# Kernel optimization log

Hardware: AMD Instinct MI355X
Metric: run time of the kernel (lower is better)

The kernel has to match this reference:

```python
import jax, jax.numpy as jnp
import numpy as np


def setup_inputs() -> dict:
    key = jax.random.key(0)
    ks = jax.random.split(key, 9)
    B, C, D = 16384, 6, 128
    NUM_ITEMS, V0, V1 = 1_000_000, 1000, 50000
    init_range = 0.5 / D
    return {
        "central_items": jax.random.randint(ks[0], (B,), 0, NUM_ITEMS),
        "side_info0": jax.random.randint(ks[1], (B,), 0, V0),
        "side_info1": jax.random.randint(ks[2], (B, 5), 0, V1),
        "context_items": jax.random.randint(ks[3], (B, C), 0, NUM_ITEMS),
        "W_item_in": jax.random.uniform(ks[4], (NUM_ITEMS, D), jnp.float32, -init_range, init_range),
        "W_item_out": jax.random.uniform(ks[5], (NUM_ITEMS, D), jnp.float32, -init_range, init_range),
        "W_weights": jax.random.normal(ks[6], (NUM_ITEMS, 3), jnp.float32),
        "W_side0": jax.random.uniform(ks[7], (V0, D), jnp.float32, -init_range, init_range),
        "W_side1": jax.random.uniform(ks[8], (V1, D), jnp.float32, -init_range, init_range),
    }


def reference(central_items, side_info0, side_info1, context_items,
              W_item_in, W_item_out, W_weights, W_side0, W_side1):
    # _emb_items: gather item + side-info embeddings
    item_embs = W_item_in[central_items]              # [B, D]
    s0 = W_side0[side_info0]                          # [B, D]
    s1 = W_side1[side_info1].mean(axis=1)             # [B, 5, D] -> [B, D] (3D mean path)
    # cat + reshape(B, -1, D) == stack along a new axis since all have width D
    embs = jnp.stack([item_embs, s0, s1], axis=1)     # [B, K=3, D]
    w = jax.nn.softmax(W_weights[central_items], axis=1)  # [B, K]
    hidden = jnp.einsum("bk,bkd->bd", w, embs)        # softmax-weighted sum, [B, D]
    # scoring: bmm(hidden[B,1,D], context[B,D,C]) -> [B, C]
    ctx = W_item_out[context_items]                   # [B, C, D]
    logits = jnp.einsum("bd,bcd->bc", hidden, ctx)    # [B, C]
    return jax.nn.sigmoid(logits)
```

## Files before the change

kernel.cpp:

```cpp
#include <hip/hip_runtime.h>
#include <math.h>


#define B_CONST 16384
#define C_CONST 6
#define D_CONST 128

__global__ __launch_bounds__(256) void eges_kernel(
    const int* __restrict__ central,
    const int* __restrict__ side0,
    const int* __restrict__ side1,
    const int* __restrict__ ctx_items,
    const float* __restrict__ W_item_in,
    const float* __restrict__ W_item_out,
    const float* __restrict__ W_weights,
    const float* __restrict__ W_side0,
    const float* __restrict__ W_side1,
    float* __restrict__ out,
    int B)
{
    const int wave = threadIdx.x >> 6;
    const int lane = threadIdx.x & 63;
    const int b = (blockIdx.x << 2) + wave;
    if (b >= B) return;

    const int ci = central[b];

    const float* wp = &W_weights[(long long)ci * 3];
    float w0 = wp[0], w1 = wp[1], w2 = wp[2];
    float m = fmaxf(w0, fmaxf(w1, w2));
    float e0 = __expf(w0 - m), e1 = __expf(w1 - m), e2 = __expf(w2 - m);
    float inv = 1.0f / (e0 + e1 + e2);
    w0 = e0 * inv; w1 = e1 * inv; w2 = e2 * inv;

    const int d = lane * 2;

    float2 item = *(const float2*)&W_item_in[(long long)ci * D_CONST + d];
    float2 s0v  = *(const float2*)&W_side0[(long long)side0[b] * D_CONST + d];

    float sx = 0.f, sy = 0.f;
    #pragma unroll
    for (int j = 0; j < 5; ++j) {
        int i1 = side1[b * 5 + j];
        float2 t = *(const float2*)&W_side1[(long long)i1 * D_CONST + d];
        sx += t.x; sy += t.y;
    }
    sx *= 0.2f; sy *= 0.2f;

    const float hx = w0 * item.x + w1 * s0v.x + w2 * sx;
    const float hy = w0 * item.y + w1 * s0v.y + w2 * sy;

    #pragma unroll
    for (int c = 0; c < C_CONST; ++c) {
        int oi = ctx_items[b * C_CONST + c];
        float2 o = *(const float2*)&W_item_out[(long long)oi * D_CONST + d];
        float p = hx * o.x + hy * o.y;
        #pragma unroll
        for (int off = 32; off >= 1; off >>= 1)
            p += __shfl_xor(p, off, 64);
        if (lane == 0)
            out[b * C_CONST + c] = 1.0f / (1.0f + __expf(-p));
    }
}

extern "C" void kernel_launch(void* const* d_in, const int* in_sizes, int n_in,
                              void* d_out, int out_size, void* d_ws, size_t ws_size,
                              hipStream_t stream) {
    const int*   central    = (const int*)d_in[0];
    const int*   side0      = (const int*)d_in[1];
    const int*   side1      = (const int*)d_in[2];
    const int*   ctx_items  = (const int*)d_in[3];
    const float* W_item_in  = (const float*)d_in[4];
    const float* W_item_out = (const float*)d_in[5];
    const float* W_weights  = (const float*)d_in[6];
    const float* W_side0    = (const float*)d_in[7];
    const float* W_side1    = (const float*)d_in[8];
    float* out = (float*)d_out;

    const int B = in_sizes[0];
    const int blocks = (B + 3) / 4;

    eges_kernel<<<blocks, 256, 0, stream>>>(
        central, side0, side1, ctx_items,
        W_item_in, W_item_out, W_weights, W_side0, W_side1,
        out, B);
}
```

Before: 25.57 us.

## Process two batch rows per wave with float4 gathers and hoisted loads

Each 64-lane wave now handles two batch rows, one per 32-lane half, and each lane loads float4 chunks instead of float2. All index loads and all six context-row gathers are issued up front, before the softmax and dot products, so more memory requests are in flight at once. The shuffle reduction shrinks to 5 steps within a half-wave. This raises register use and depends on ctx_items rows being 8-byte aligned for the int2 loads, which holds since each row is 6 ints.

```diff
diff --git a/kernel.cpp b/kernel.cpp
--- a/kernel.cpp
+++ b/kernel.cpp
@@ -2,7 +2,6 @@
 #include <math.h>
 
 
-#define B_CONST 16384
 #define C_CONST 6
 #define D_CONST 128
 
@@ -21,45 +20,61 @@
 {
     const int wave = threadIdx.x >> 6;
     const int lane = threadIdx.x & 63;
-    const int b = (blockIdx.x << 2) + wave;
+    const int half = lane >> 5;
+    const int l    = lane & 31;
+    const int b = blockIdx.x * 8 + wave * 2 + half;
     if (b >= B) return;
 
-    const int ci = central[b];
+    const int d = l * 4;
+
+    const int ci  = central[b];
+    const int s0i = side0[b];
+
+    int s1idx[5];
+    #pragma unroll
+    for (int j = 0; j < 5; ++j) s1idx[j] = side1[b * 5 + j];
+
+    const int2 c01 = *(const int2*)&ctx_items[b * 6 + 0];
+    const int2 c23 = *(const int2*)&ctx_items[b * 6 + 2];
+    const int2 c45 = *(const int2*)&ctx_items[b * 6 + 4];
+    const int cidx[6] = { c01.x, c01.y, c23.x, c23.y, c45.x, c45.y };
+
+    const float4 item = *(const float4*)&W_item_in[(long long)ci  * D_CONST + d];
+    const float4 s0v  = *(const float4*)&W_side0 [(long long)s0i * D_CONST + d];
+
+    float4 sacc = make_float4(0.f, 0.f, 0.f, 0.f);
+    #pragma unroll
+    for (int j = 0; j < 5; ++j) {
+        float4 t = *(const float4*)&W_side1[(long long)s1idx[j] * D_CONST + d];
+        sacc.x += t.x; sacc.y += t.y; sacc.z += t.z; sacc.w += t.w;
+    }
+
+    float4 o[6];
+    #pragma unroll
+    for (int c = 0; c < 6; ++c)
+        o[c] = *(const float4*)&W_item_out[(long long)cidx[c] * D_CONST + d];
 
     const float* wp = &W_weights[(long long)ci * 3];
     float w0 = wp[0], w1 = wp[1], w2 = wp[2];
-    float m = fmaxf(w0, fmaxf(w1, w2));
-    float e0 = __expf(w0 - m), e1 = __expf(w1 - m), e2 = __expf(w2 - m);
-    float inv = 1.0f / (e0 + e1 + e2);
+    const float m = fmaxf(w0, fmaxf(w1, w2));
+    const float e0 = __expf(w0 - m), e1 = __expf(w1 - m), e2 = __expf(w2 - m);
+    const float inv = 1.0f / (e0 + e1 + e2);
     w0 = e0 * inv; w1 = e1 * inv; w2 = e2 * inv;
 
-    const int d = lane * 2;
-
-    float2 item = *(const float2*)&W_item_in[(long long)ci * D_CONST + d];
-    float2 s0v  = *(const float2*)&W_side0[(long long)side0[b] * D_CONST + d];
-
-    float sx = 0.f, sy = 0.f;
-    #pragma unroll
-    for (int j = 0; j < 5; ++j) {
-        int i1 = side1[b * 5 + j];
-        float2 t = *(const float2*)&W_side1[(long long)i1 * D_CONST + d];
-        sx += t.x; sy += t.y;
-    }
-    sx *= 0.2f; sy *= 0.2f;
-
-    const float hx = w0 * item.x + w1 * s0v.x + w2 * sx;
-    const float hy = w0 * item.y + w1 * s0v.y + w2 * sy;
+    float4 h;
+    h.x = w0 * item.x + w1 * s0v.x + w2 * (sacc.x * 0.2f);
+    h.y = w0 * item.y + w1 * s0v.y + w2 * (sacc.y * 0.2f);
+    h.z = w0 * item.z + w1 * s0v.z + w2 * (sacc.z * 0.2f);
+    h.w = w0 * item.w + w1 * s0v.w + w2 * (sacc.w * 0.2f);
 
     #pragma unroll
-    for (int c = 0; c < C_CONST; ++c) {
-        int oi = ctx_items[b * C_CONST + c];
-        float2 o = *(const float2*)&W_item_out[(long long)oi * D_CONST + d];
-        float p = hx * o.x + hy * o.y;
+    for (int c = 0; c < 6; ++c) {
+        float p = h.x * o[c].x + h.y * o[c].y + h.z * o[c].z + h.w * o[c].w;
         #pragma unroll
-        for (int off = 32; off >= 1; off >>= 1)
+        for (int off = 16; off >= 1; off >>= 1)
             p += __shfl_xor(p, off, 64);
-        if (lane == 0)
-            out[b * C_CONST + c] = 1.0f / (1.0f + __expf(-p));
+        if (l == 0)
+            out[b * 6 + c] = 1.0f / (1.0f + __expf(-p));
     }
 }
 
@@ -78,7 +93,7 @@
     float* out = (float*)d_out;
 
     const int B = in_sizes[0];
-    const int blocks = (B + 3) / 4;
+    const int blocks = (B + 7) / 8;
 
     eges_kernel<<<blocks, 256, 0, stream>>>(
         central, side0, side1, ctx_items,
```

Result: faster. 22.58 us (-11.7%).
